# Optimization experiments

Hardware: AMD Instinct MI355X
Metric: run time of the kernel (lower is better)

Reference implementation:

```python
import jax, jax.numpy as jnp
import numpy as np

# Module hyperparameters (match init_kwargs)
T0, Z0, T1, Z1, K, S, ROUTING = 4, 16, 8, 16, 5, 1, 3
PAD = 2  # hard-coded padding=2 in the torch module
N, H, W_SP = 4, 128, 128


def setup_inputs() -> dict:
    key = jax.random.key(0)
    k1, k2 = jax.random.split(key)
    u = jax.random.normal(k1, (N, T0, Z0, H, W_SP), dtype=jnp.float32)
    # t_0 independent Conv2d(z_0 -> t_1*z_1, k, s, padding=2, bias=False) weights
    W = jax.random.normal(k2, (T0, T1 * Z1, Z0, K, K), dtype=jnp.float32) * 0.05
    return {"u": u, "W": W}


def _squash(p):
    # squash along last (z_1) axis, matching torch: p_norm = sqrt(|p|^2 + 1e-9)
    n2 = jnp.sum(p * p, axis=-1, keepdims=True)
    n = jnp.sqrt(n2 + 1e-9)
    return n2 / (1.0 + n2) * p / n


def _capsule_convs(u, W):
    # t_0 independent convs == one grouped conv with feature_group_count=t_0
    n, t0, z0, h, w = u.shape
    x = u.reshape(n, t0 * z0, h, w)
    wk = W.reshape(t0 * T1 * Z1, z0, K, K)
    y = jax.lax.conv_general_dilated(
        x, wk, window_strides=(S, S), padding=[(PAD, PAD), (PAD, PAD)],
        dimension_numbers=("NCHW", "OIHW", "NCHW"), feature_group_count=t0)
    h1, w1 = y.shape[2], y.shape[3]
    # [N, t0*t1*z1, H1, W1] -> u_hat [t0, N, H1, W1, t1, z1]
    y = y.reshape(n, t0, T1, Z1, h1, w1)
    return jnp.transpose(y, (1, 0, 4, 5, 2, 3))


def _routing(u_hat):
    t0, n, h, w, t1, z1 = u_hat.shape
    dt = u_hat.dtype
    b = jnp.zeros((t0, n, t1, h, w), dt)  # NCHW layout per capsule type
    neg_inf = jnp.array(-jnp.inf, dt)
    zero = jnp.array(0.0, dt)
    win = (1, 1, 1, K, K)
    ones = (1, 1, 1, 1, 1)
    pad = [(0, 0), (0, 0), (0, 0), (PAD, PAD), (PAD, PAD)]
    v = None
    for d in range(ROUTING):
        uh = jax.lax.stop_gradient(u_hat) if d < ROUTING - 1 else u_hat
        # stability max: max_pool2d(k,1,pad=2) (pads with -inf) then max over t1
        b_max = jax.lax.reduce_window(b, neg_inf, jax.lax.max, win, ones, pad)
        b_max = jnp.max(b_max, axis=2, keepdims=True)
        c = jnp.exp(b - b_max)  # [t0, N, t1, H, W]
        # conv2d_same with ones kernel [1,t1,k,k] == channel-sum then kxk box-sum
        sum_c = jax.lax.reduce_window(jnp.sum(c, axis=2, keepdims=True), zero,
                                      jax.lax.add, win, ones, pad)
        r = c / sum_c                                   # [t0, N, t1, H, W]
        r = jnp.transpose(r, (0, 1, 3, 4, 2))[..., None]  # [t0,N,H,W,t1,1]
        p = jnp.sum(r * uh, axis=0)                     # [N, H, W, t1, z1]
        v = _squash(p)
        # NOTE: the original torch code computes b + (u_hat*v).sum(4) into a
        # list `b_t_list_` that is never assigned back, so b stays zero across
        # iterations. We faithfully reproduce that (no b update).
    return jnp.transpose(v, (0, 3, 4, 1, 2))  # [N, t1, z1, H, W]


def reference(u, W):
    return _routing(_capsule_convs(u, W))
```

## Files before the change

### kernel.cpp

```cpp
#include <hip/hip_runtime.h>
#include <hip/hip_bf16.h>


#define CO 128

typedef __attribute__((ext_vector_type(8))) short bf16x8;
typedef __attribute__((ext_vector_type(4))) float f32x4;

__global__ __launch_bounds__(256) void k_reorder(const float* __restrict__ Wsrc,
                                                 ushort* __restrict__ Wr2b) {
    int idx = blockIdx.x * 256 + threadIdx.x;
    int ci = idx & 63;
    int r  = idx >> 6;
    int co = r & 127;
    int kk = r >> 7;
    int t0 = ci >> 4, z0 = ci & 15;
    __hip_bfloat16 bb = __float2bfloat16(Wsrc[((t0 * CO + co) * 16 + z0) * 25 + kk]);
    int cg = co >> 6, ni = (co >> 4) & 3, m16 = co & 15;
    int ks = ci >> 5, q = (ci >> 3) & 3, j = ci & 7;
    int oi = ((((kk * 2 + cg) * 2 + ks) * 4 + ni) << 9) + ((q * 16 + m16) << 3) + j;
    Wr2b[oi] = *(ushort*)&bb;
}

__global__ __launch_bounds__(256) void k_caps(const float* __restrict__ u,
                                              const ushort* __restrict__ Wr2b,
                                              float* __restrict__ out) {
    __shared__ ushort As[240 * 68];

    int tid = threadIdx.x;
    int bid = blockIdx.x;
    int bx = bid & 7, by = (bid >> 3) & 15, n = bid >> 7;
    int h0 = by * 8, w0 = bx * 16;

    int lane = tid & 63, wid = tid >> 6;
    int rg = wid >> 1;
    int cg = wid & 1;
    int wm4  = rg * 4;
    int wn64 = cg * 64;
    int q = lane >> 4, m16 = lane & 15;

    const ushort* wp = Wr2b + ((size_t)cg * 4096) + lane * 8;

    bf16x8 bA[8], bB[8];
#define LOADB(dst, kk2)                                                  \
    {                                                                    \
        _Pragma("unroll") for (int ks_ = 0; ks_ < 2; ++ks_)              \
            _Pragma("unroll") for (int ni_ = 0; ni_ < 4; ++ni_)          \
                dst[ks_ * 4 + ni_] = *(const bf16x8*)(                   \
                    wp + (size_t)(kk2) * 8192 + (ks_ * 4 + ni_) * 512);  \
    }

    LOADB(bA, 0);

    for (int i = tid; i < 1920; i += 256) {
        int p = i >> 3, c = i & 7;
        int rr = p / 20, cc = p - rr * 20;
        int hh = h0 + rr - 2, ww = w0 + cc - 2;
        bf16x8 v = {};
        if (((unsigned)hh < 128u) & ((unsigned)ww < 128u)) {
            const float* up = u + (size_t)n * (64 * 128 * 128) + (size_t)hh * 128 + ww;
#pragma unroll
            for (int j = 0; j < 8; ++j) {
                __hip_bfloat16 bb = __float2bfloat16(up[(size_t)(c * 8 + j) * 16384]);
                v[j] = *(ushort*)&bb;
            }
        }
        *(bf16x8*)&As[p * 68 + c * 8] = v;
    }
    __syncthreads();
    LOADB(bB, 1);

    const ushort* ap = As + (wm4 * 20 + m16) * 68 + q * 8;

    f32x4 acc[4][4] = {};

#pragma unroll
    for (int kk = 0; kk < 25; ++kk) {
        const int kh = kk / 5, kw = kk % 5;
#pragma unroll
        for (int ks = 0; ks < 2; ++ks) {
            bf16x8 a[4];
#pragma unroll
            for (int mi = 0; mi < 4; ++mi)
                a[mi] = *(const bf16x8*)(ap + ((mi + kh) * 20 + kw) * 68 + ks * 32);
#pragma unroll
            for (int mi = 0; mi < 4; ++mi)
#pragma unroll
                for (int ni = 0; ni < 4; ++ni)
                    acc[mi][ni] = __builtin_amdgcn_mfma_f32_16x16x32_bf16(
                        a[mi], (kk & 1) ? bB[ks * 4 + ni] : bA[ks * 4 + ni],
                        acc[mi][ni], 0, 0, 0);
        }
        if (kk < 23) {
            if (kk & 1) { LOADB(bB, kk + 2); }
            else        { LOADB(bA, kk + 2); }
        }
    }
#undef LOADB

#pragma unroll
    for (int mi = 0; mi < 4; ++mi) {
        int h = h0 + wm4 + mi;
        int hlo = h - 2; if (hlo < 0) hlo = 0;
        int hhi = h + 2; if (hhi > 127) hhi = 127;
        float cnth = (float)(hhi - hlo + 1);
#pragma unroll
        for (int ni = 0; ni < 4; ++ni) {
            f32x4 cv = acc[mi][ni];
            float ov[4];
#pragma unroll
            for (int reg = 0; reg < 4; ++reg) {
                int w = w0 + q * 4 + reg;
                int wlo = w - 2; if (wlo < 0) wlo = 0;
                int whi = w + 2; if (whi > 127) whi = 127;
                float s = 1.f / (8.f * cnth * (float)(whi - wlo + 1));
                float pv = cv[reg] * s;
                float n2 = pv * pv;
                n2 += __shfl_xor(n2, 1);
                n2 += __shfl_xor(n2, 2);
                n2 += __shfl_xor(n2, 4);
                n2 += __shfl_xor(n2, 8);
                float fac = n2 / ((1.f + n2) * sqrtf(n2 + 1e-9f));
                ov[reg] = pv * fac;
            }
            int co = wn64 + ni * 16 + m16;
            *(float4*)(out + (((size_t)(n * CO + co)) << 14) + h * 128 + w0 + q * 4) =
                make_float4(ov[0], ov[1], ov[2], ov[3]);
        }
    }
}

extern "C" void kernel_launch(void* const* d_in, const int* in_sizes, int n_in,
                              void* d_out, int out_size, void* d_ws, size_t ws_size,
                              hipStream_t stream) {
    const float* u    = (const float*)d_in[0];
    const float* Wsrc = (const float*)d_in[1];
    float* out = (float*)d_out;
    ushort* Wr2b = (ushort*)d_ws;

    k_reorder<<<800, 256, 0, stream>>>(Wsrc, Wr2b);
    k_caps<<<512, 256, 0, stream>>>(u, Wr2b, out);
}
```

Measured before the change: 117.1 us.

## Pre-transpose input to NHWC bf16 in prep kernel and double-buffer LDS A fragments

The weight-reorder kernel becomes a combined prep kernel that also transposes u from NCHW fp32 into an NHWC bf16 buffer through an LDS tile. The main kernel then fills its halo tile with one 16-byte load per pixel chunk instead of eight strided scalar fp32 loads. The main kernel also double-buffers its A-operand LDS reads one kernel tap ahead of the MFMAs. The cost is an extra full pass over u with a write and re-read of the bf16 copy, plus higher register pressure from the added A buffers.

```diff
diff --git a/kernel.cpp b/kernel.cpp
--- a/kernel.cpp
+++ b/kernel.cpp
@@ -7,22 +7,59 @@
 typedef __attribute__((ext_vector_type(8))) short bf16x8;
 typedef __attribute__((ext_vector_type(4))) float f32x4;
 
-__global__ __launch_bounds__(256) void k_reorder(const float* __restrict__ Wsrc,
-                                                 ushort* __restrict__ Wr2b) {
-    int idx = blockIdx.x * 256 + threadIdx.x;
-    int ci = idx & 63;
-    int r  = idx >> 6;
-    int co = r & 127;
-    int kk = r >> 7;
-    int t0 = ci >> 4, z0 = ci & 15;
-    __hip_bfloat16 bb = __float2bfloat16(Wsrc[((t0 * CO + co) * 16 + z0) * 25 + kk]);
-    int cg = co >> 6, ni = (co >> 4) & 3, m16 = co & 15;
-    int ks = ci >> 5, q = (ci >> 3) & 3, j = ci & 7;
-    int oi = ((((kk * 2 + cg) * 2 + ks) * 4 + ni) << 9) + ((q * 16 + m16) << 3) + j;
-    Wr2b[oi] = *(ushort*)&bb;
+__global__ __launch_bounds__(256) void k_prep(const float* __restrict__ u,
+                                              const float* __restrict__ Wsrc,
+                                              ushort* __restrict__ ut,
+                                              ushort* __restrict__ Wr2b) {
+    __shared__ float lt[64][65];
+    int b = blockIdx.x;
+    int t = threadIdx.x;
+    if (b < 800) {
+        int idx = b * 256 + t;
+        int ci = idx & 63;
+        int r  = idx >> 6;
+        int co = r & 127;
+        int kk = r >> 7;
+        int t0 = ci >> 4, z0 = ci & 15;
+        __hip_bfloat16 bb = __float2bfloat16(Wsrc[((t0 * CO + co) * 16 + z0) * 25 + kk]);
+        int cg = co >> 6, ni = (co >> 4) & 3, m16 = co & 15;
+        int ks = ci >> 5, q = (ci >> 3) & 3, j = ci & 7;
+        int oi = ((((kk * 2 + cg) * 2 + ks) * 4 + ni) << 9) + ((q * 16 + m16) << 3) + j;
+        Wr2b[oi] = *(ushort*)&bb;
+        return;
+    }
+    b -= 800;
+    int wc = b & 1; int nh = b >> 1; int h = nh & 127; int n = nh >> 7;
+    int w0 = wc * 64;
+    int ciL = t >> 4;
+    int wl  = (t & 15) * 4;
+    const float* up = u + (size_t)n * (64 * 128 * 128) + h * 128 + w0;
+#pragma unroll
+    for (int p = 0; p < 4; ++p) {
+        int ci = p * 16 + ciL;
+        float4 v = *(const float4*)(up + (size_t)ci * 16384 + wl);
+        lt[wl + 0][ci] = v.x;
+        lt[wl + 1][ci] = v.y;
+        lt[wl + 2][ci] = v.z;
+        lt[wl + 3][ci] = v.w;
+    }
+    __syncthreads();
+    ushort* op = ut + (((size_t)(n * 128 + h)) * 128 + w0) * 64;
+#pragma unroll
+    for (int p = 0; p < 2; ++p) {
+        int item = p * 256 + t;
+        int c8 = item & 7, w2 = item >> 3;
+        bf16x8 vv;
+#pragma unroll
+        for (int j = 0; j < 8; ++j) {
+            __hip_bfloat16 bb = __float2bfloat16(lt[w2][c8 * 8 + j]);
+            vv[j] = *(ushort*)&bb;
+        }
+        *(bf16x8*)(op + (size_t)w2 * 64 + c8 * 8) = vv;
+    }
 }
 
-__global__ __launch_bounds__(256) void k_caps(const float* __restrict__ u,
+__global__ __launch_bounds__(256) void k_caps(const ushort* __restrict__ ut,
                                               const ushort* __restrict__ Wr2b,
                                               float* __restrict__ out) {
     __shared__ ushort As[240 * 68];
@@ -57,14 +94,8 @@
         int rr = p / 20, cc = p - rr * 20;
         int hh = h0 + rr - 2, ww = w0 + cc - 2;
         bf16x8 v = {};
-        if (((unsigned)hh < 128u) & ((unsigned)ww < 128u)) {
-            const float* up = u + (size_t)n * (64 * 128 * 128) + (size_t)hh * 128 + ww;
-#pragma unroll
-            for (int j = 0; j < 8; ++j) {
-                __hip_bfloat16 bb = __float2bfloat16(up[(size_t)(c * 8 + j) * 16384]);
-                v[j] = *(ushort*)&bb;
-            }
-        }
+        if (((unsigned)hh < 128u) & ((unsigned)ww < 128u))
+            v = *(const bf16x8*)(ut + (((size_t)(n * 128 + hh)) * 128 + ww) * 64 + c * 8);
         *(bf16x8*)&As[p * 68 + c * 8] = v;
     }
     __syncthreads();
@@ -72,30 +103,42 @@
 
     const ushort* ap = As + (wm4 * 20 + m16) * 68 + q * 8;
 
+#define LOADA(dst, kk2)                                                     \
+    {                                                                       \
+        const int kh_ = (kk2) / 5, kw_ = (kk2) % 5;                         \
+        _Pragma("unroll") for (int ks_ = 0; ks_ < 2; ++ks_)                 \
+            _Pragma("unroll") for (int mi_ = 0; mi_ < 4; ++mi_)             \
+                dst[ks_ * 4 + mi_] = *(const bf16x8*)(                      \
+                    ap + ((mi_ + kh_) * 20 + kw_) * 68 + ks_ * 32);         \
+    }
+
+    bf16x8 aA[8], aB[8];
+    LOADA(aA, 0);
+
     f32x4 acc[4][4] = {};
 
 #pragma unroll
     for (int kk = 0; kk < 25; ++kk) {
-        const int kh = kk / 5, kw = kk % 5;
+        if (kk < 24) {
+            if (kk & 1) { LOADA(aA, kk + 1); }
+            else        { LOADA(aB, kk + 1); }
+        }
+        const bf16x8* av = (kk & 1) ? aB : aA;
+        const bf16x8* bv = (kk & 1) ? bB : bA;
 #pragma unroll
-        for (int ks = 0; ks < 2; ++ks) {
-            bf16x8 a[4];
-#pragma unroll
-            for (int mi = 0; mi < 4; ++mi)
-                a[mi] = *(const bf16x8*)(ap + ((mi + kh) * 20 + kw) * 68 + ks * 32);
+        for (int ks = 0; ks < 2; ++ks)
 #pragma unroll
             for (int mi = 0; mi < 4; ++mi)
 #pragma unroll
                 for (int ni = 0; ni < 4; ++ni)
                     acc[mi][ni] = __builtin_amdgcn_mfma_f32_16x16x32_bf16(
-                        a[mi], (kk & 1) ? bB[ks * 4 + ni] : bA[ks * 4 + ni],
-                        acc[mi][ni], 0, 0, 0);
-        }
+                        av[ks * 4 + mi], bv[ks * 4 + ni], acc[mi][ni], 0, 0, 0);
         if (kk < 23) {
             if (kk & 1) { LOADB(bB, kk + 2); }
             else        { LOADB(bA, kk + 2); }
         }
     }
+#undef LOADA
 #undef LOADB
 
 #pragma unroll
@@ -137,7 +180,8 @@
     const float* Wsrc = (const float*)d_in[1];
     float* out = (float*)d_out;
     ushort* Wr2b = (ushort*)d_ws;
+    ushort* ut   = (ushort*)((char*)d_ws + 409600);
 
-    k_reorder<<<800, 256, 0, stream>>>(Wsrc, Wr2b);
-    k_caps<<<512, 256, 0, stream>>>(u, Wr2b, out);
+    k_prep<<<1824, 256, 0, stream>>>(u, Wsrc, ut, Wr2b);
+    k_caps<<<512, 256, 0, stream>>>(ut, Wr2b, out);
 }
```

Result: faster. 110.1 us (-6.0%).
